# Kernel optimization log

Measured on AMD Instinct MI355X. Metric: run time of the kernel, lower is better.

The kernel has to match this reference:

```python
import jax, jax.numpy as jnp
import numpy as np

K = 20          # neighbors
T = 3           # time steps
GW = 10.0       # surrogate-gradient width
EPS = 1e-5      # batchnorm eps


def _knn_idx(f, k):
    # f: (B, N, C). torch code maximizes -||xi-xj||^2 via topk.
    x2 = jnp.sum(f * f, axis=-1)                          # (B, N)
    inner = jnp.einsum('bnc,bmc->bnm', f, f)              # (B, N, N)
    neg_d = 2.0 * inner - x2[:, :, None] - x2[:, None, :]
    return jax.lax.top_k(neg_d, k)[1]                     # (B, N, k)


def _graph_feature(f, k):
    # f: (B, N, C) -> (B, N, k, 2C) = cat(neighbor - center, neighbor)
    idx = _knn_idx(f, k)
    nb = jax.vmap(lambda ft, ix: ft[ix])(f, idx)          # (B, N, k, C)
    return jnp.concatenate([nb - f[:, :, None, :], nb], axis=-1)


def _bn(x, g, b, axes):
    # training-mode batchnorm (batch statistics), channel-last
    m = jnp.mean(x, axis=axes, keepdims=True)
    v = jnp.var(x, axis=axes, keepdims=True)
    return (x - m) * jax.lax.rsqrt(v + EPS) * g + b


def _lrelu(x):
    return jnp.where(x >= 0, x, 0.2 * x)


def _spike(x):
    # surrogate value + straight-through hard spike (training-mode detach trick)
    xc = jnp.clip(x, -10.0, 10.0)
    soft = 0.5 * jnp.exp(-0.5 * xc * xc) / np.sqrt(2.0 * np.pi) + 0.5 * jax.nn.sigmoid(GW * xc)
    hard = (x > 0).astype(x.dtype)
    return soft + jax.lax.stop_gradient(hard - soft)


def _lif(x, mem, thr, ref, md, ta, rd, tb):
    md = jnp.clip(md, 0.1, 0.99)
    ta = jnp.clip(ta, 0.001, 0.1)
    rd = jnp.clip(rd, 0.1, 0.95)
    x = x * (ref <= 0).astype(x.dtype)
    mem = mem * md * (1.0 - ref) + x
    s = _spike(mem - thr)
    mem = mem * (1.0 - s)
    ref = ref * rd + s
    thr = tb + (thr + ta * s - tb) * 0.95
    return s, mem, thr, ref


def _forward(x, W0, g0, b0, W1, g1, b1, W2, g2, b2, W3, g3, b3, Wm, gm, bm,
             l0md, l0ta, l0rd, l0tb, l1md, l1ta, l1rd, l1tb,
             l2md, l2ta, l2rd, l2tb, l3md, l3ta, l3rd, l3tb,
             lfmd, lfta, lfrd, lftb, tw):
    f0 = jnp.transpose(x, (0, 2, 1))                      # (B, N, 3)
    convs = [(W0, g0, b0), (W1, g1, b1), (W2, g2, b2), (W3, g3, b3)]
    lifs = [(l0md, l0ta, l0rd, l0tb), (l1md, l1ta, l1rd, l1tb),
            (l2md, l2ta, l2rd, l2tb), (l3md, l3ta, l3rd, l3tb)]
    states = [None] * 4
    pooled = []
    for t in range(T):
        cur = f0
        feats = []
        for i in range(4):
            gf = _graph_feature(cur, K)                   # (B, N, k, 2C)
            h = jnp.einsum('bnkc,oc->bnko', gf, convs[i][0])  # 1x1 conv
            h = _lrelu(_bn(h, convs[i][1], convs[i][2], (0, 1, 2)))
            h = jnp.max(h, axis=2)                        # max over k -> (B, N, O)
            md, ta, rd, tb = lifs[i]
            if states[i] is None:
                mem = jnp.zeros_like(h)
                thr = jnp.broadcast_to(tb, h.shape).astype(h.dtype)
                ref = jnp.zeros_like(h)
            else:
                # state manager detaches persisted states between calls
                mem, thr, ref = (jax.lax.stop_gradient(s) for s in states[i])
            s, mem, thr, ref = _lif(h, mem, thr, ref, md, ta, rd, tb)
            states[i] = (mem, thr, ref)
            feats.append(s)
            cur = s
        cat = jnp.concatenate(feats, axis=-1)             # (B, N, 960)
        agg = _lrelu(_bn(jnp.einsum('bnc,oc->bno', cat, Wm), gm, bm, (0, 1)))
        pooled.append(jnp.max(agg, axis=1))               # global max pool -> (B, 512)
    tf = jnp.stack(pooled, axis=0)                        # (T, B, 512)
    out = jnp.einsum('t,tbf->bf', jax.nn.softmax(tw), tf)
    mem = jnp.zeros_like(out)
    thr = jnp.broadcast_to(lftb, out.shape).astype(out.dtype)
    ref = jnp.zeros_like(out)
    s, _, _, _ = _lif(out, mem, thr, ref, lfmd, lfta, lfrd, lftb)
    return s


def setup_inputs() -> dict:
    key = jax.random.key(0)
    ks = iter(jax.random.split(key, 64))
    B, N = 2, 1024
    d = {}
    d['x'] = jax.random.normal(next(ks), (B, 3, N), jnp.float32)
    dims = [(64, 6), (128, 128), (256, 256), (512, 512)]  # (out, in) for 1x1 convs
    for i, (o, c) in enumerate(dims):
        d[f'W{i}'] = jax.random.normal(next(ks), (o, c), jnp.float32) / np.sqrt(c)
        d[f'g{i}'] = 1.0 + 0.1 * jax.random.normal(next(ks), (o,), jnp.float32)
        d[f'b{i}'] = 0.1 * jax.random.normal(next(ks), (o,), jnp.float32)
    d['Wm'] = jax.random.normal(next(ks), (512, 960), jnp.float32) / np.sqrt(960.0)
    d['gm'] = 1.0 + 0.1 * jax.random.normal(next(ks), (512,), jnp.float32)
    d['bm'] = 0.1 * jax.random.normal(next(ks), (512,), jnp.float32)
    for name, c in [('l0', 64), ('l1', 128), ('l2', 256), ('l3', 512), ('lf', 512)]:
        d[name + 'md'] = jnp.full((c,), 0.9, jnp.float32) + 0.02 * jax.random.normal(next(ks), (c,), jnp.float32)
        d[name + 'ta'] = jnp.full((c,), 0.01, jnp.float32) + 0.002 * jax.random.normal(next(ks), (c,), jnp.float32)
        d[name + 'rd'] = jnp.full((c,), 0.5, jnp.float32) + 0.02 * jax.random.normal(next(ks), (c,), jnp.float32)
        d[name + 'tb'] = jnp.ones((c,), jnp.float32) + 0.05 * jax.random.normal(next(ks), (c,), jnp.float32)
    d['tw'] = 1.0 + 0.1 * jax.random.normal(next(ks), (T,), jnp.float32)
    return d


def reference(x, W0, g0, b0, W1, g1, b1, W2, g2, b2, W3, g3, b3, Wm, gm, bm,
              l0md, l0ta, l0rd, l0tb, l1md, l1ta, l1rd, l1tb,
              l2md, l2ta, l2rd, l2tb, l3md, l3ta, l3rd, l3tb,
              lfmd, lfta, lfrd, lftb, tw):
    return _forward(x, W0, g0, b0, W1, g1, b1, W2, g2, b2, W3, g3, b3, Wm, gm, bm,
                    l0md, l0ta, l0rd, l0tb, l1md, l1ta, l1rd, l1tb,
                    l2md, l2ta, l2rd, l2tb, l3md, l3ta, l3rd, l3tb,
                    lfmd, lfta, lfrd, lftb, tw)
```

## Files before the change

### kernel.cpp

```cpp
#include <hip/hip_runtime.h>
#include <math.h>

#define NPTS 1024
#define BB 2
#define KNN 20
#define ROWS 2048
#define CATC 960
#define TT 3
typedef unsigned long long ull;

__device__ __forceinline__ float lrelu_f(float x){ return x >= 0.f ? x : 0.2f*x; }

__device__ __forceinline__ void gemm_dev(const float* __restrict__ A, int lda,
    const float* __restrict__ B, int ldb, float* __restrict__ C, int ldc,
    int K, int kb, int bm, int bn, int tid, float* sm)
{
  float (*As)[68] = (float(*)[68])sm;
  float (*Bs)[68] = (float(*)[68])(sm + 16*68);
  const int tx = tid & 15, ty = tid >> 4;
  const int lr = tid >> 2, kq = tid & 3;
  float acc[4][4] = {};
  if ((K & 15) == 0) {
    const float* pA = A + (size_t)(bm+lr)*lda + kb + kq*4;
    const float* pB = B + (size_t)(bn+lr)*ldb + kb + kq*4;
    float4 av = *(const float4*)pA;
    float4 bv = *(const float4*)pB;
    for (int k0 = 0; k0 < K; k0 += 16) {
      As[kq*4+0][lr]=av.x; As[kq*4+1][lr]=av.y; As[kq*4+2][lr]=av.z; As[kq*4+3][lr]=av.w;
      Bs[kq*4+0][lr]=bv.x; Bs[kq*4+1][lr]=bv.y; Bs[kq*4+2][lr]=bv.z; Bs[kq*4+3][lr]=bv.w;
      __syncthreads();
      if (k0 + 16 < K) {
        av = *(const float4*)(pA + k0 + 16);
        bv = *(const float4*)(pB + k0 + 16);
      }
#pragma unroll
      for (int kk = 0; kk < 16; ++kk) {
        float4 a4 = *(const float4*)&As[kk][ty*4];
        float4 b4 = *(const float4*)&Bs[kk][tx*4];
        float ar[4]={a4.x,a4.y,a4.z,a4.w}, br[4]={b4.x,b4.y,b4.z,b4.w};
#pragma unroll
        for (int i=0;i<4;++i)
#pragma unroll
          for (int j=0;j<4;++j) acc[i][j]=fmaf(ar[i],br[j],acc[i][j]);
      }
      __syncthreads();
    }
  } else {
    for (int k0 = 0; k0 < K; k0 += 16) {
#pragma unroll
      for (int e=0;e<4;++e){
        int gk = k0 + kq*4 + e;
        As[kq*4+e][lr] = (gk<K)? A[(size_t)(bm+lr)*lda+kb+gk] : 0.f;
        Bs[kq*4+e][lr] = (gk<K)? B[(size_t)(bn+lr)*ldb+kb+gk] : 0.f;
      }
      __syncthreads();
#pragma unroll
      for (int kk = 0; kk < 16; ++kk) {
        float4 a4 = *(const float4*)&As[kk][ty*4];
        float4 b4 = *(const float4*)&Bs[kk][tx*4];
        float ar[4]={a4.x,a4.y,a4.z,a4.w}, br[4]={b4.x,b4.y,b4.z,b4.w};
#pragma unroll
        for (int i=0;i<4;++i)
#pragma unroll
          for (int j=0;j<4;++j) acc[i][j]=fmaf(ar[i],br[j],acc[i][j]);
      }
      __syncthreads();
    }
  }
#pragma unroll
  for (int i=0;i<4;++i){
    float4 v; v.x=acc[i][0]; v.y=acc[i][1]; v.z=acc[i][2]; v.w=acc[i][3];
    *(float4*)&C[(size_t)(bm+ty*4+i)*ldc + bn + tx*4] = v;
  }
}

template<int W>
__device__ __forceinline__ void knn_wave(const ull* __restrict__ pk, int* __restrict__ idx,
                                         int row, int lane)
{
  const int n = row & (NPTS-1), b = row >> 10;
  const ull* pb = pk + (size_t)b*NPTS*W;
  ull cw[W]; int pn = 0;
#pragma unroll
  for (int w=0; w<W; ++w){ cw[w] = pb[(size_t)n*W + w]; pn += __popcll(cw[w]); }
  unsigned keys[16];
#pragma unroll 4
  for (int i=0;i<16;++i){
    int m = lane + (i<<6);
    int inner=0, pm=0;
#pragma unroll
    for (int w=0;w<W;++w){
      ull rm = pb[(size_t)m*W + w];
      inner += __popcll(rm & cw[w]);
      pm    += __popcll(rm);
    }
    int d = 2*inner - pn - pm;
    keys[i] = ((unsigned)(d+1024)<<11) | (unsigned)(NPTS-1-m);
  }
  unsigned lmax = keys[0];
#pragma unroll
  for (int i=1;i<16;++i) lmax = keys[i]>lmax ? keys[i] : lmax;
  unsigned mywin = 0;
  for (int s=0;s<KNN;++s){
    unsigned v = lmax;
#pragma unroll
    for (int off=1; off<64; off<<=1){ unsigned o = __shfl_xor(v, off, 64); if (o>v) v=o; }
    if (lane == s) mywin = (unsigned)(NPTS-1) - (v & 0x7FFu);
    if (lmax == v){
#pragma unroll
      for (int i=0;i<16;++i) if (keys[i]==v) keys[i]=0u;
      lmax = keys[0];
#pragma unroll
      for (int i=1;i<16;++i) lmax = keys[i]>lmax ? keys[i] : lmax;
    }
  }
  if (lane < KNN) idx[(size_t)row*KNN + lane] = (int)mywin;
}

__device__ __forceinline__ void knn0_wave(const float* __restrict__ x, const float* __restrict__ x2,
                                          int* __restrict__ idx, int row, int lane)
{
  const int n = row & (NPTS-1), b = row >> 10;
  const float* xb = x + (size_t)b*3*NPTS;
  float fn0 = xb[n], fn1 = xb[NPTS+n], fn2 = xb[2*NPTS+n];
  float x2n = x2[row];
  ull keys[16];
#pragma unroll 4
  for (int i=0;i<16;++i){
    int m = lane + (i<<6);
    float inner = __fadd_rn(__fadd_rn(__fmul_rn(fn0, xb[m]), __fmul_rn(fn1, xb[NPTS+m])),
                            __fmul_rn(fn2, xb[2*NPTS+m]));
    float v = __fsub_rn(__fsub_rn(__fmul_rn(2.f, inner), x2n), x2[(b<<10)+m]);
    unsigned u = __float_as_uint(v);
    u = (u & 0x80000000u) ? ~u : (u | 0x80000000u);
    keys[i] = ((ull)u << 32) | (unsigned)(NPTS-1-m);
  }
  ull lmax = keys[0];
#pragma unroll
  for (int i=1;i<16;++i) lmax = keys[i]>lmax ? keys[i] : lmax;
  unsigned mywin = 0;
  for (int s=0;s<KNN;++s){
    ull v = lmax;
#pragma unroll
    for (int off=1; off<64; off<<=1){ ull o = __shfl_xor(v, off, 64); if (o>v) v=o; }
    if (lane == s) mywin = (unsigned)(NPTS-1) - (unsigned)(v & 0xFFFFFFFFull);
    if (lmax == v){
#pragma unroll
      for (int i=0;i<16;++i) if (keys[i]==v) keys[i]=0ull;
      lmax = keys[0];
#pragma unroll
      for (int i=1;i<16;++i) lmax = keys[i]>lmax ? keys[i] : lmax;
    }
  }
  if (lane < KNN) idx[(size_t)row*KNN + lane] = (int)mywin;
}

__device__ __forceinline__ void bnlif_dev(int i, int oShift,
    const float* __restrict__ hmax, const double* __restrict__ S1, const double* __restrict__ S2,
    const float* __restrict__ g, const float* __restrict__ bb,
    const float* __restrict__ pmd, const float* __restrict__ pta,
    const float* __restrict__ prd, const float* __restrict__ ptb,
    float* __restrict__ stM, float* __restrict__ stT, float* __restrict__ stR,
    float* __restrict__ sout, int offOut, ull* __restrict__ pk, int init, int laneTid)
{
  int O = 1 << oShift;
  int bn = i >> oShift;
  int o  = i & (O - 1);
  double cnt = (double)ROWS * (double)KNN;
  double mu = S1[o] / cnt;
  double vv = S2[o] / cnt - mu*mu;
  float mean = (float)mu;
  float inv  = 1.f / sqrtf((float)vv + 1e-5f);
  float h = hmax[i];
  h = ((h - mean) * inv) * g[o] + bb[o];
  h = lrelu_f(h);
  float md = fminf(fmaxf(pmd[o], 0.1f), 0.99f);
  float ta = fminf(fmaxf(pta[o], 0.001f), 0.1f);
  float rd = fminf(fmaxf(prd[o], 0.1f), 0.95f);
  float tb = ptb[o];
  float M, T, R;
  if (init) { M = 0.f; T = tb; R = 0.f; }
  else      { M = stM[i]; T = stT[i]; R = stR[i]; }
  float xv = (R <= 0.f) ? h : 0.f;
  M = M * md * (1.f - R) + xv;
  float sp = (M - T > 0.f) ? 1.f : 0.f;
  M = M * (1.f - sp);
  R = R * rd + sp;
  T = tb + (T + ta*sp - tb) * 0.95f;
  stM[i] = M; stT[i] = T; stR[i] = R;
  sout[(size_t)bn*CATC + offOut + o] = sp;
  ull ball = __ballot(sp != 0.f);
  if ((laneTid & 63) == 0) pk[i >> 6] = ball;
}

__device__ __forceinline__ void aggfin_dev(const float* __restrict__ pA, const float* __restrict__ pB,
    const float* __restrict__ gm, const float* __restrict__ bmv, float* __restrict__ pooled,
    int o, int tid, char* smraw)
{
  double* sd1 = (double*)smraw; double* sd2 = sd1 + 256;
  float* sm0 = (float*)(sd2 + 256); float* sm1 = sm0 + 256;
  double s1=0.0, s2=0.0; float m0=-INFINITY, m1=-INFINITY;
  for (int r=tid; r<ROWS; r+=256){
    float v = __fadd_rn(pA[(size_t)r*512+o], pB[(size_t)r*512+o]);
    s1 += (double)v; s2 += (double)v*(double)v;
    if (r < NPTS) m0 = fmaxf(m0, v); else m1 = fmaxf(m1, v);
  }
  sd1[tid]=s1; sd2[tid]=s2; sm0[tid]=m0; sm1[tid]=m1;
  __syncthreads();
  for (int off=128; off>0; off>>=1){
    if (tid<off){
      sd1[tid]+=sd1[tid+off]; sd2[tid]+=sd2[tid+off];
      sm0[tid]=fmaxf(sm0[tid],sm0[tid+off]);
      sm1[tid]=fmaxf(sm1[tid],sm1[tid+off]);
    }
    __syncthreads();
  }
  if (tid==0){
    double mean = sd1[0]/(double)ROWS;
    float var = (float)(sd2[0]/(double)ROWS - mean*mean);
    float m = (float)mean;
    float inv = 1.f/sqrtf(var + 1e-5f);
    pooled[o]       = lrelu_f(((sm0[0]-m)*inv)*gm[o] + bmv[o]);
    pooled[512 + o] = lrelu_f(((sm1[0]-m)*inv)*gm[o] + bmv[o]);
  }
}

__device__ __forceinline__ void wcat_dev(const float* __restrict__ W, float* __restrict__ out,
                                         int O, int C, int i)
{
  if (i >= 2*O*C) return;
  int r = i / C, c = i - r*C;
  out[i] = (r < O) ? __fadd_rn(W[(size_t)r*2*C + c], W[(size_t)r*2*C + C + c])
                   : W[(size_t)(r-O)*2*C + c];
}

__global__ __launch_bounds__(256) void k_setup(const float* __restrict__ x,
    float* __restrict__ f0, float* __restrict__ x2,
    const float* W0, const float* W1, const float* W2, const float* W3,
    float* wc0, float* wc1, float* wc2, float* wc3, double* S12_0)
{
  int bid = blockIdx.x, tid = threadIdx.x;
  if (bid < 24) {
    int i = bid*256 + tid;
    int b = i / 3072, rem = i - b*3072, n = rem/3, c = rem - n*3;
    f0[i] = x[(size_t)b*3072 + c*NPTS + n];
  } else if (bid < 32) {
    int r = (bid-24)*256 + tid;
    int b = r >> 10, n = r & (NPTS-1);
    const float* xb = x + (size_t)b*3072;
    float a0=xb[n], a1=xb[NPTS+n], a2=xb[2*NPTS+n];
    x2[r] = __fadd_rn(__fadd_rn(__fmul_rn(a0,a0),__fmul_rn(a1,a1)),__fmul_rn(a2,a2));
  } else if (bid < 33) {
    for (int j=tid; j<1024; j+=256) S12_0[j]=0.0;
  } else if (bid < 35) {
    int i = (bid-33)*256+tid; wcat_dev(W0, wc0, 64, 3, i);
  } else if (bid < 99) {
    int i = (bid-35)*256+tid; wcat_dev(W1, wc1, 128, 64, i);
  } else if (bid < 355) {
    int i = (bid-99)*256+tid; wcat_dev(W2, wc2, 256, 128, i);
  } else {
    int i = (bid-355)*256+tid; wcat_dev(W3, wc3, 512, 256, i);
  }
}

__global__ __launch_bounds__(256) void k_nt0v2(const float* __restrict__ x, const float* __restrict__ x2,
    int* __restrict__ idx0, const float* __restrict__ f0, const float* __restrict__ wc0,
    float* __restrict__ AB)
{
  __shared__ __align__(16) float sm[2*16*68];
  int bid = blockIdx.x, tid = threadIdx.x;
  if (bid < 512) {
    knn0_wave(x, x2, idx0, bid*4 + (tid>>6), tid & 63);
  } else {
    int id = bid - 512;
    gemm_dev(f0, 3, wc0, 3, AB, 128, 3, 0, (id>>1)*64, (id&1)*64, tid, sm);
  }
}

template<int W>
__global__ __launch_bounds__(256) void k_knnconv2(const ull* __restrict__ pk, int* __restrict__ idx,
    double* __restrict__ S12, const float* __restrict__ Ain, const float* __restrict__ Bw,
    float* __restrict__ AB, int twoO, int K, int ntn)
{
  __shared__ __align__(16) float sm[2*16*68];
  int bid = blockIdx.x, tid = threadIdx.x;
  if (bid < 512) {
    if (bid == 0) { for (int j=tid; j<1024; j+=256) S12[j]=0.0; }
    knn_wave<W>(pk, idx, bid*4 + (tid>>6), tid & 63);
  } else {
    int id = bid - 512;
    int tm = id / ntn, tn = id - tm*ntn;
    gemm_dev(Ain, CATC, Bw, K, AB, twoO, K, 0, tm*64, tn*64, tid, sm);
  }
}

__global__ __launch_bounds__(256) void k_agg(const float* __restrict__ scat, const float* __restrict__ Wm,
    float* __restrict__ aggA, float* __restrict__ aggB)
{
  __shared__ __align__(16) float sm[2*16*68];
  int id = blockIdx.x;
  int part = id >> 8, tl = id & 255, tm = tl >> 3, tn = tl & 7;
  gemm_dev(scat, CATC, Wm, CATC, part ? aggB : aggA, 512, 480, part*480,
           tm*64, tn*64, threadIdx.x, sm);
}

__global__ __launch_bounds__(256) void k_lif0fin(
    const float* __restrict__ hmax0, const double* __restrict__ S1_0, const double* __restrict__ S2_0,
    const float* g, const float* bb, const float* pmd, const float* pta,
    const float* prd, const float* ptb,
    float* stM, float* stT, float* stR, float* scc, ull* pk0, int init,
    const float* aggA, const float* aggB, const float* gm, const float* bmv, float* pooled)
{
  __shared__ __align__(16) char sm[6144];
  int bid = blockIdx.x, tid = threadIdx.x;
  if (bid < 512) {
    bnlif_dev(bid*256+tid, 6, hmax0, S1_0, S2_0, g, bb, pmd, pta, prd, ptb,
              stM, stT, stR, scc, 0, pk0, init, tid);
  } else {
    aggfin_dev(aggA, aggB, gm, bmv, pooled, bid-512, tid, sm);
  }
}

__global__ __launch_bounds__(256) void k_gather(const float* __restrict__ AB, int O,
    const int* __restrict__ idx, float* __restrict__ hmax,
    double* __restrict__ S1, double* __restrict__ S2)
{
  int base = blockIdx.x * 8;
  __shared__ int sidx[8*KNN];
  for (int i = threadIdx.x; i < 8*KNN; i += blockDim.x)
    sidx[i] = idx[(size_t)base*KNN + i];
  __syncthreads();
  int twoO = 2*O;
  for (int o = threadIdx.x; o < O; o += blockDim.x) {
    double ts1 = 0.0, ts2 = 0.0;
    for (int r = 0; r < 8; ++r) {
      int bn = base + r;
      int b = bn >> 10;
      float bc = AB[(size_t)bn*twoO + O + o];
      float mx = -INFINITY;
      double s1 = 0.0, s2 = 0.0;
#pragma unroll
      for (int k = 0; k < KNN; ++k) {
        int m = sidx[r*KNN + k];
        float a = AB[((size_t)(b*NPTS + m))*twoO + o];
        mx = fmaxf(mx, a);
        s1 += (double)a;
        s2 += (double)a * (double)a;
      }
      hmax[(size_t)bn*O + o] = mx - bc;
      ts1 += s1 - (double)KNN * (double)bc;
      ts2 += s2 - 2.0*(double)bc*s1 + (double)KNN*(double)bc*(double)bc;
    }
    atomicAdd(&S1[o], ts1);
    atomicAdd(&S2[o], ts2);
  }
}

__global__ __launch_bounds__(256) void k_bnlif(const float* __restrict__ hmax, int oShift,
    const double* __restrict__ S1, const double* __restrict__ S2,
    const float* g, const float* bb, const float* pmd, const float* pta,
    const float* prd, const float* ptb,
    float* stM, float* stT, float* stR, float* scc, int offOut, ull* pk, int init)
{
  bnlif_dev(blockIdx.x*256 + threadIdx.x, oShift, hmax, S1, S2, g, bb, pmd, pta, prd, ptb,
            stM, stT, stR, scc, offOut, pk, init, threadIdx.x);
}

__global__ __launch_bounds__(256) void k_aggfin(const float* __restrict__ aggA,
    const float* __restrict__ aggB, const float* gm, const float* bmv, float* pooled)
{
  __shared__ __align__(16) char sm[6144];
  aggfin_dev(aggA, aggB, gm, bmv, pooled, blockIdx.x, threadIdx.x, sm);
}

__global__ __launch_bounds__(256) void k_final(const float* __restrict__ pooled,
    const float* __restrict__ tw, const float* __restrict__ lftb, float* __restrict__ out)
{
  int i = blockIdx.x*256 + threadIdx.x;
  if (i >= BB*512) return;
  int b = i / 512, o = i - b*512;
  float t0 = tw[0], t1 = tw[1], t2 = tw[2];
  float mx = fmaxf(t0, fmaxf(t1, t2));
  float e0 = expf(t0-mx), e1 = expf(t1-mx), e2 = expf(t2-mx);
  float den = e0 + e1 + e2;
  float v = (e0/den)*pooled[(0*BB+b)*512+o]
          + (e1/den)*pooled[(1*BB+b)*512+o]
          + (e2/den)*pooled[(2*BB+b)*512+o];
  out[i] = (v - lftb[o] > 0.f) ? 1.f : 0.f;
}

extern "C" void kernel_launch(void* const* d_in, const int* in_sizes, int n_in,
                              void* d_out, int out_size, void* d_ws, size_t ws_size,
                              hipStream_t stream)
{
  (void)in_sizes; (void)n_in; (void)out_size; (void)ws_size;
  const float* x = (const float*)d_in[0];
  const float* Wl[4] = {(const float*)d_in[1],(const float*)d_in[4],(const float*)d_in[7],(const float*)d_in[10]};
  const float* gl[4] = {(const float*)d_in[2],(const float*)d_in[5],(const float*)d_in[8],(const float*)d_in[11]};
  const float* bl[4] = {(const float*)d_in[3],(const float*)d_in[6],(const float*)d_in[9],(const float*)d_in[12]};
  const float* Wm = (const float*)d_in[13];
  const float* gm = (const float*)d_in[14];
  const float* bm = (const float*)d_in[15];
  const float* lp[5][4];
  for (int l = 0; l < 5; ++l)
    for (int q = 0; q < 4; ++q)
      lp[l][q] = (const float*)d_in[16 + l*4 + q];
  const float* tw = (const float*)d_in[36];

  char* pw = (char*)d_ws;
  auto alloc = [&](size_t bytes)->char* {
    char* r = pw; pw += (bytes + 255) & ~(size_t)255; return r;
  };
  float* f0     = (float*)alloc((size_t)ROWS*3*sizeof(float));
  float* x2     = (float*)alloc((size_t)ROWS*sizeof(float));
  int*   idx0   = (int*)  alloc((size_t)ROWS*KNN*sizeof(int));
  int*   idxS   = (int*)  alloc((size_t)ROWS*KNN*sizeof(int));
  float* AB     = (float*)alloc((size_t)ROWS*1024*sizeof(float));
  float* hmax0  = (float*)alloc((size_t)ROWS*64*sizeof(float));
  float* hmaxS  = (float*)alloc((size_t)ROWS*512*sizeof(float));
  float* aggA   = (float*)alloc((size_t)ROWS*512*sizeof(float));
  float* scat   = (float*)alloc((size_t)ROWS*CATC*sizeof(float));
  double* S12_0 = (double*)alloc(1024*sizeof(double));
  double* S12   = (double*)alloc(1024*sizeof(double));
  float* pooled = (float*)alloc((size_t)TT*BB*512*sizeof(float));
  ull* pkb[4];
  int Wn[4] = {1, 2, 4, 8};
  for (int i = 0; i < 4; ++i)
    pkb[i] = (ull*)alloc((size_t)ROWS*Wn[i]*sizeof(ull));

  int Cin[4]   = {3, 64, 128, 256};
  int Oo[4]    = {64, 128, 256, 512};
  int oSh[4]   = {6, 7, 8, 9};
  int offIn[4] = {0, 0, 64, 192};
  int offOut[4]= {0, 64, 192, 448};
  float *wcat[4], *stM[4], *stT[4], *stR[4];
  for (int i = 0; i < 4; ++i) {
    wcat[i] = (float*)alloc((size_t)2*Oo[i]*Cin[i]*sizeof(float));
    stM[i]  = (float*)alloc((size_t)ROWS*Oo[i]*sizeof(float));
    stT[i]  = (float*)alloc((size_t)ROWS*Oo[i]*sizeof(float));
    stR[i]  = (float*)alloc((size_t)ROWS*Oo[i]*sizeof(float));
  }
  double* S1_0 = S12_0; double* S2_0 = S12_0 + 512;
  double* S1 = S12;     double* S2 = S12 + 512;
  float* aggB = hmaxS;

  k_setup<<<1379, 256, 0, stream>>>(x, f0, x2, Wl[0], Wl[1], Wl[2], Wl[3],
                                    wcat[0], wcat[1], wcat[2], wcat[3], S12_0);
  k_nt0v2<<<576, 256, 0, stream>>>(x, x2, idx0, f0, wcat[0], AB);
  k_gather<<<256, 256, 0, stream>>>(AB, 64, idx0, hmax0, S1_0, S2_0);

  for (int t = 0; t < TT; ++t) {
    int init = (t == 0) ? 1 : 0;
    if (t > 0)
      k_agg<<<512, 256, 0, stream>>>(scat, Wm, aggA, aggB);
    k_lif0fin<<<(t > 0 ? 1024 : 512), 256, 0, stream>>>(
        hmax0, S1_0, S2_0, gl[0], bl[0],
        lp[0][0], lp[0][1], lp[0][2], lp[0][3],
        stM[0], stT[0], stR[0], scat, pkb[0], init,
        aggA, aggB, gm, bm, pooled + (t > 0 ? (size_t)(t-1)*BB*512 : 0));
    for (int i = 1; i < 4; ++i) {
      int C = Cin[i], O = Oo[i];
      int twoO = 2*O, ntn = twoO/64, nConv = 32*ntn;
      const float* fin = scat + offIn[i];
      switch (Wn[i-1]) {
        case 1: k_knnconv2<1><<<512+nConv, 256, 0, stream>>>(pkb[0], idxS, S12, fin, wcat[i], AB, twoO, C, ntn); break;
        case 2: k_knnconv2<2><<<512+nConv, 256, 0, stream>>>(pkb[1], idxS, S12, fin, wcat[i], AB, twoO, C, ntn); break;
        default: k_knnconv2<4><<<512+nConv, 256, 0, stream>>>(pkb[2], idxS, S12, fin, wcat[i], AB, twoO, C, ntn); break;
      }
      k_gather<<<256, 256, 0, stream>>>(AB, O, idxS, hmaxS, S1, S2);
      k_bnlif<<<(ROWS*O)/256, 256, 0, stream>>>(
          hmaxS, oSh[i], S1, S2, gl[i], bl[i],
          lp[i][0], lp[i][1], lp[i][2], lp[i][3],
          stM[i], stT[i], stR[i], scat, offOut[i], pkb[i], init);
    }
  }
  k_agg<<<512, 256, 0, stream>>>(scat, Wm, aggA, aggB);
  k_aggfin<<<512, 256, 0, stream>>>(aggA, aggB, gm, bm, pooled + (size_t)2*BB*512);
  k_final<<<4, 256, 0, stream>>>(pooled, tw, lp[4][3], (float*)d_out);
}
```

Measured before the change: 542.3 us.

## Use bf16 MFMA with three-way weight splitting for spike-input GEMMs

Replaces the fp32 shared-memory GEMMs for layers 1-3 and the aggregation projection with MFMA 16x16x32 bf16 instructions. Weights are split into three bf16 terms at setup, and spike activations, which are exactly 0 or 1, are stored as bf16, so precision is kept close to fp32. The spike concat buffer shrinks to half size. In exchange, setup work grows, each output needs three MFMA passes, operands are loaded straight from global memory without LDS staging, and the C stores are strided.

```diff
diff --git a/kernel.cpp b/kernel.cpp
--- a/kernel.cpp
+++ b/kernel.cpp
@@ -8,8 +8,18 @@
 #define CATC 960
 #define TT 3
 typedef unsigned long long ull;
+typedef __attribute__((ext_vector_type(8))) short bf16x8;
+typedef __attribute__((ext_vector_type(4))) float f32x4;
 
 __device__ __forceinline__ float lrelu_f(float x){ return x >= 0.f ? x : 0.2f*x; }
+
+__device__ __forceinline__ unsigned short f2bf(float f){
+  unsigned u = __float_as_uint(f);
+  return (unsigned short)((u + 0x7FFFu + ((u >> 16) & 1u)) >> 16);
+}
+__device__ __forceinline__ float bf2f(unsigned short h){
+  return __uint_as_float(((unsigned)h) << 16);
+}
 
 __device__ __forceinline__ void gemm_dev(const float* __restrict__ A, int lda,
     const float* __restrict__ B, int ldb, float* __restrict__ C, int ldc,
@@ -20,58 +30,64 @@
   const int tx = tid & 15, ty = tid >> 4;
   const int lr = tid >> 2, kq = tid & 3;
   float acc[4][4] = {};
-  if ((K & 15) == 0) {
-    const float* pA = A + (size_t)(bm+lr)*lda + kb + kq*4;
-    const float* pB = B + (size_t)(bn+lr)*ldb + kb + kq*4;
-    float4 av = *(const float4*)pA;
-    float4 bv = *(const float4*)pB;
-    for (int k0 = 0; k0 < K; k0 += 16) {
-      As[kq*4+0][lr]=av.x; As[kq*4+1][lr]=av.y; As[kq*4+2][lr]=av.z; As[kq*4+3][lr]=av.w;
-      Bs[kq*4+0][lr]=bv.x; Bs[kq*4+1][lr]=bv.y; Bs[kq*4+2][lr]=bv.z; Bs[kq*4+3][lr]=bv.w;
-      __syncthreads();
-      if (k0 + 16 < K) {
-        av = *(const float4*)(pA + k0 + 16);
-        bv = *(const float4*)(pB + k0 + 16);
-      }
-#pragma unroll
-      for (int kk = 0; kk < 16; ++kk) {
-        float4 a4 = *(const float4*)&As[kk][ty*4];
-        float4 b4 = *(const float4*)&Bs[kk][tx*4];
-        float ar[4]={a4.x,a4.y,a4.z,a4.w}, br[4]={b4.x,b4.y,b4.z,b4.w};
-#pragma unroll
-        for (int i=0;i<4;++i)
-#pragma unroll
-          for (int j=0;j<4;++j) acc[i][j]=fmaf(ar[i],br[j],acc[i][j]);
-      }
-      __syncthreads();
-    }
-  } else {
-    for (int k0 = 0; k0 < K; k0 += 16) {
-#pragma unroll
-      for (int e=0;e<4;++e){
-        int gk = k0 + kq*4 + e;
-        As[kq*4+e][lr] = (gk<K)? A[(size_t)(bm+lr)*lda+kb+gk] : 0.f;
-        Bs[kq*4+e][lr] = (gk<K)? B[(size_t)(bn+lr)*ldb+kb+gk] : 0.f;
-      }
-      __syncthreads();
-#pragma unroll
-      for (int kk = 0; kk < 16; ++kk) {
-        float4 a4 = *(const float4*)&As[kk][ty*4];
-        float4 b4 = *(const float4*)&Bs[kk][tx*4];
-        float ar[4]={a4.x,a4.y,a4.z,a4.w}, br[4]={b4.x,b4.y,b4.z,b4.w};
-#pragma unroll
-        for (int i=0;i<4;++i)
-#pragma unroll
-          for (int j=0;j<4;++j) acc[i][j]=fmaf(ar[i],br[j],acc[i][j]);
-      }
-      __syncthreads();
-    }
+  for (int k0 = 0; k0 < K; k0 += 16) {
+#pragma unroll
+    for (int e=0;e<4;++e){
+      int gk = k0 + kq*4 + e;
+      As[kq*4+e][lr] = (gk<K)? A[(size_t)(bm+lr)*lda+kb+gk] : 0.f;
+      Bs[kq*4+e][lr] = (gk<K)? B[(size_t)(bn+lr)*ldb+kb+gk] : 0.f;
+    }
+    __syncthreads();
+#pragma unroll
+    for (int kk = 0; kk < 16; ++kk) {
+      float4 a4 = *(const float4*)&As[kk][ty*4];
+      float4 b4 = *(const float4*)&Bs[kk][tx*4];
+      float ar[4]={a4.x,a4.y,a4.z,a4.w}, br[4]={b4.x,b4.y,b4.z,b4.w};
+#pragma unroll
+      for (int i=0;i<4;++i)
+#pragma unroll
+        for (int j=0;j<4;++j) acc[i][j]=fmaf(ar[i],br[j],acc[i][j]);
+    }
+    __syncthreads();
   }
 #pragma unroll
   for (int i=0;i<4;++i){
     float4 v; v.x=acc[i][0]; v.y=acc[i][1]; v.z=acc[i][2]; v.w=acc[i][3];
     *(float4*)&C[(size_t)(bm+ty*4+i)*ldc + bn + tx*4] = v;
   }
+}
+
+__device__ __forceinline__ void mfma_dev(const short* __restrict__ A, int lda,
+    const short* __restrict__ B3, size_t sStride, int ldb,
+    float* __restrict__ C, int ldc, int K, int kb, int bm, int bn, int tid)
+{
+  const int wave = tid >> 6, lane = tid & 63;
+  const int wm = (wave >> 1) << 5, wn = (wave & 1) << 5;
+  const int rr = lane & 15, kq = (lane >> 4) << 3;
+  f32x4 acc[2][2] = {};
+  const short* Ap = A + (size_t)(bm + wm + rr)*lda + kb + kq;
+  const short* Bp = B3 + (size_t)(bn + wn + rr)*ldb + kb + kq;
+  for (int k0 = 0; k0 < K; k0 += 32) {
+    bf16x8 a0 = *(const bf16x8*)(Ap + k0);
+    bf16x8 a1 = *(const bf16x8*)(Ap + (size_t)16*lda + k0);
+#pragma unroll
+    for (int s = 0; s < 3; ++s) {
+      bf16x8 b0 = *(const bf16x8*)(Bp + (size_t)s*sStride + k0);
+      bf16x8 b1 = *(const bf16x8*)(Bp + (size_t)s*sStride + (size_t)16*ldb + k0);
+      acc[0][0] = __builtin_amdgcn_mfma_f32_16x16x32_bf16(a0, b0, acc[0][0], 0, 0, 0);
+      acc[0][1] = __builtin_amdgcn_mfma_f32_16x16x32_bf16(a0, b1, acc[0][1], 0, 0, 0);
+      acc[1][0] = __builtin_amdgcn_mfma_f32_16x16x32_bf16(a1, b0, acc[1][0], 0, 0, 0);
+      acc[1][1] = __builtin_amdgcn_mfma_f32_16x16x32_bf16(a1, b1, acc[1][1], 0, 0, 0);
+    }
+  }
+  const int drb = (lane >> 4) << 2;
+#pragma unroll
+  for (int i = 0; i < 2; ++i)
+#pragma unroll
+    for (int j = 0; j < 2; ++j)
+#pragma unroll
+      for (int t = 0; t < 4; ++t)
+        C[(size_t)(bm + wm + i*16 + drb + t)*ldc + bn + wn + j*16 + rr] = acc[i][j][t];
 }
 
 template<int W>
@@ -161,7 +177,7 @@
     const float* __restrict__ pmd, const float* __restrict__ pta,
     const float* __restrict__ prd, const float* __restrict__ ptb,
     float* __restrict__ stM, float* __restrict__ stT, float* __restrict__ stR,
-    float* __restrict__ sout, int offOut, ull* __restrict__ pk, int init, int laneTid)
+    short* __restrict__ sout, int offOut, ull* __restrict__ pk, int init, int laneTid)
 {
   int O = 1 << oShift;
   int bn = i >> oShift;
@@ -182,13 +198,13 @@
   if (init) { M = 0.f; T = tb; R = 0.f; }
   else      { M = stM[i]; T = stT[i]; R = stR[i]; }
   float xv = (R <= 0.f) ? h : 0.f;
+  float sp = (M * md * (1.f - R) + xv - T > 0.f) ? 1.f : 0.f;
   M = M * md * (1.f - R) + xv;
-  float sp = (M - T > 0.f) ? 1.f : 0.f;
   M = M * (1.f - sp);
   R = R * rd + sp;
   T = tb + (T + ta*sp - tb) * 0.95f;
   stM[i] = M; stT[i] = T; stR[i] = R;
-  sout[(size_t)bn*CATC + offOut + o] = sp;
+  sout[(size_t)bn*CATC + offOut + o] = (sp != 0.f) ? (short)0x3F80 : (short)0;
   ull ball = __ballot(sp != 0.f);
   if ((laneTid & 63) == 0) pk[i >> 6] = ball;
 }
@@ -225,19 +241,25 @@
   }
 }
 
-__device__ __forceinline__ void wcat_dev(const float* __restrict__ W, float* __restrict__ out,
-                                         int O, int C, int i)
-{
-  if (i >= 2*O*C) return;
-  int r = i / C, c = i - r*C;
-  out[i] = (r < O) ? __fadd_rn(W[(size_t)r*2*C + c], W[(size_t)r*2*C + C + c])
-                   : W[(size_t)(r-O)*2*C + c];
+__device__ __forceinline__ void wsplit_dev(float w, short* dst, size_t NK, size_t e){
+  unsigned short h1 = f2bf(w); float f1 = bf2f(h1);
+  float r1 = w - f1;
+  unsigned short h2 = f2bf(r1); float f2v = bf2f(h2);
+  unsigned short h3 = f2bf(r1 - f2v);
+  dst[e] = (short)h1; dst[NK + e] = (short)h2; dst[2*NK + e] = (short)h3;
+}
+__device__ __forceinline__ void wcatsplit_dev(const float* __restrict__ W, short* __restrict__ dst,
+                                              int O, int C, size_t e){
+  int rr = (int)(e / C), cc = (int)(e - (size_t)rr*C);
+  float w = (rr < O) ? __fadd_rn(W[(size_t)rr*2*C + cc], W[(size_t)rr*2*C + C + cc])
+                     : W[(size_t)(rr-O)*2*C + cc];
+  wsplit_dev(w, dst, (size_t)2*O*C, e);
 }
 
 __global__ __launch_bounds__(256) void k_setup(const float* __restrict__ x,
     float* __restrict__ f0, float* __restrict__ x2,
-    const float* W0, const float* W1, const float* W2, const float* W3,
-    float* wc0, float* wc1, float* wc2, float* wc3, double* S12_0)
+    const float* W0, const float* W1, const float* W2, const float* W3, const float* Wm,
+    float* wc0, short* wcH1, short* wcH2, short* wcH3, short* WmH, double* S12_0)
 {
   int bid = blockIdx.x, tid = threadIdx.x;
   if (bid < 24) {
@@ -253,14 +275,16 @@
   } else if (bid < 33) {
     for (int j=tid; j<1024; j+=256) S12_0[j]=0.0;
   } else if (bid < 35) {
-    int i = (bid-33)*256+tid; wcat_dev(W0, wc0, 64, 3, i);
-  } else if (bid < 99) {
-    int i = (bid-35)*256+tid; wcat_dev(W1, wc1, 128, 64, i);
-  } else if (bid < 355) {
-    int i = (bid-99)*256+tid; wcat_dev(W2, wc2, 256, 128, i);
-  } else {
-    int i = (bid-355)*256+tid; wcat_dev(W3, wc3, 512, 256, i);
-  }
+    int i = (bid-33)*256+tid;
+    if (i < 2*64*3){
+      int r = i/3, c = i-r*3;
+      wc0[i] = (r<64) ? __fadd_rn(W0[(size_t)r*6+c], W0[(size_t)r*6+3+c])
+                      : W0[(size_t)(r-64)*6+c];
+    }
+  } else if (bid < 99)   { wcatsplit_dev(W1, wcH1, 128,  64, (size_t)(bid-35)*256+tid); }
+  else if (bid < 355)    { wcatsplit_dev(W2, wcH2, 256, 128, (size_t)(bid-99)*256+tid); }
+  else if (bid < 1379)   { wcatsplit_dev(W3, wcH3, 512, 256, (size_t)(bid-355)*256+tid); }
+  else                   { size_t e = (size_t)(bid-1379)*256+tid; wsplit_dev(Wm[e], WmH, (size_t)512*960, e); }
 }
 
 __global__ __launch_bounds__(256) void k_nt0v2(const float* __restrict__ x, const float* __restrict__ x2,
@@ -278,11 +302,10 @@
 }
 
 template<int W>
-__global__ __launch_bounds__(256) void k_knnconv2(const ull* __restrict__ pk, int* __restrict__ idx,
-    double* __restrict__ S12, const float* __restrict__ Ain, const float* __restrict__ Bw,
-    float* __restrict__ AB, int twoO, int K, int ntn)
-{
-  __shared__ __align__(16) float sm[2*16*68];
+__global__ __launch_bounds__(256) void k_knnmfma(const ull* __restrict__ pk, int* __restrict__ idx,
+    double* __restrict__ S12, const short* __restrict__ Ain, const short* __restrict__ B3,
+    size_t sStride, float* __restrict__ AB, int twoO, int K, int ntn)
+{
   int bid = blockIdx.x, tid = threadIdx.x;
   if (bid < 512) {
     if (bid == 0) { for (int j=tid; j<1024; j+=256) S12[j]=0.0; }
@@ -290,25 +313,24 @@
   } else {
     int id = bid - 512;
     int tm = id / ntn, tn = id - tm*ntn;
-    gemm_dev(Ain, CATC, Bw, K, AB, twoO, K, 0, tm*64, tn*64, tid, sm);
-  }
-}
-
-__global__ __launch_bounds__(256) void k_agg(const float* __restrict__ scat, const float* __restrict__ Wm,
-    float* __restrict__ aggA, float* __restrict__ aggB)
-{
-  __shared__ __align__(16) float sm[2*16*68];
+    mfma_dev(Ain, CATC, B3, sStride, K, AB, twoO, K, 0, tm*64, tn*64, tid);
+  }
+}
+
+__global__ __launch_bounds__(256) void k_aggmfma(const short* __restrict__ scatH,
+    const short* __restrict__ WmH, float* __restrict__ aggA, float* __restrict__ aggB)
+{
   int id = blockIdx.x;
   int part = id >> 8, tl = id & 255, tm = tl >> 3, tn = tl & 7;
-  gemm_dev(scat, CATC, Wm, CATC, part ? aggB : aggA, 512, 480, part*480,
-           tm*64, tn*64, threadIdx.x, sm);
+  mfma_dev(scatH, CATC, WmH, (size_t)512*960, 960, part ? aggB : aggA, 512,
+           480, part*480, tm*64, tn*64, threadIdx.x);
 }
 
 __global__ __launch_bounds__(256) void k_lif0fin(
     const float* __restrict__ hmax0, const double* __restrict__ S1_0, const double* __restrict__ S2_0,
     const float* g, const float* bb, const float* pmd, const float* pta,
     const float* prd, const float* ptb,
-    float* stM, float* stT, float* stR, float* scc, ull* pk0, int init,
+    float* stM, float* stT, float* stR, short* scc, ull* pk0, int init,
     const float* aggA, const float* aggB, const float* gm, const float* bmv, float* pooled)
 {
   __shared__ __align__(16) char sm[6144];
@@ -360,7 +382,7 @@
     const double* __restrict__ S1, const double* __restrict__ S2,
     const float* g, const float* bb, const float* pmd, const float* pta,
     const float* prd, const float* ptb,
-    float* stM, float* stT, float* stR, float* scc, int offOut, ull* pk, int init)
+    float* stM, float* stT, float* stR, short* scc, int offOut, ull* pk, int init)
 {
   bnlif_dev(blockIdx.x*256 + threadIdx.x, oShift, hmax, S1, S2, g, bb, pmd, pta, prd, ptb,
             stM, stT, stR, scc, offOut, pk, init, threadIdx.x);
@@ -419,7 +441,7 @@
   float* hmax0  = (float*)alloc((size_t)ROWS*64*sizeof(float));
   float* hmaxS  = (float*)alloc((size_t)ROWS*512*sizeof(float));
   float* aggA   = (float*)alloc((size_t)ROWS*512*sizeof(float));
-  float* scat   = (float*)alloc((size_t)ROWS*CATC*sizeof(float));
+  short* scatH  = (short*)alloc((size_t)ROWS*CATC*sizeof(short));
   double* S12_0 = (double*)alloc(1024*sizeof(double));
   double* S12   = (double*)alloc(1024*sizeof(double));
   float* pooled = (float*)alloc((size_t)TT*BB*512*sizeof(float));
@@ -433,9 +455,14 @@
   int oSh[4]   = {6, 7, 8, 9};
   int offIn[4] = {0, 0, 64, 192};
   int offOut[4]= {0, 64, 192, 448};
-  float *wcat[4], *stM[4], *stT[4], *stR[4];
+  float* wc0 = (float*)alloc((size_t)2*64*3*sizeof(float));
+  short* wcH[4];
+  wcH[1] = (short*)alloc((size_t)3*256*64*sizeof(short));
+  wcH[2] = (short*)alloc((size_t)3*512*128*sizeof(short));
+  wcH[3] = (short*)alloc((size_t)3*1024*256*sizeof(short));
+  short* WmH = (short*)alloc((size_t)3*512*960*sizeof(short));
+  float *stM[4], *stT[4], *stR[4];
   for (int i = 0; i < 4; ++i) {
-    wcat[i] = (float*)alloc((size_t)2*Oo[i]*Cin[i]*sizeof(float));
     stM[i]  = (float*)alloc((size_t)ROWS*Oo[i]*sizeof(float));
     stT[i]  = (float*)alloc((size_t)ROWS*Oo[i]*sizeof(float));
     stR[i]  = (float*)alloc((size_t)ROWS*Oo[i]*sizeof(float));
@@ -444,37 +471,38 @@
   double* S1 = S12;     double* S2 = S12 + 512;
   float* aggB = hmaxS;
 
-  k_setup<<<1379, 256, 0, stream>>>(x, f0, x2, Wl[0], Wl[1], Wl[2], Wl[3],
-                                    wcat[0], wcat[1], wcat[2], wcat[3], S12_0);
-  k_nt0v2<<<576, 256, 0, stream>>>(x, x2, idx0, f0, wcat[0], AB);
+  k_setup<<<3299, 256, 0, stream>>>(x, f0, x2, Wl[0], Wl[1], Wl[2], Wl[3], Wm,
+                                    wc0, wcH[1], wcH[2], wcH[3], WmH, S12_0);
+  k_nt0v2<<<576, 256, 0, stream>>>(x, x2, idx0, f0, wc0, AB);
   k_gather<<<256, 256, 0, stream>>>(AB, 64, idx0, hmax0, S1_0, S2_0);
 
   for (int t = 0; t < TT; ++t) {
     int init = (t == 0) ? 1 : 0;
     if (t > 0)
-      k_agg<<<512, 256, 0, stream>>>(scat, Wm, aggA, aggB);
+      k_aggmfma<<<512, 256, 0, stream>>>(scatH, WmH, aggA, aggB);
     k_lif0fin<<<(t > 0 ? 1024 : 512), 256, 0, stream>>>(
         hmax0, S1_0, S2_0, gl[0], bl[0],
         lp[0][0], lp[0][1], lp[0][2], lp[0][3],
-        stM[0], stT[0], stR[0], scat, pkb[0], init,
+        stM[0], stT[0], stR[0], scatH, pkb[0], init,
         aggA, aggB, gm, bm, pooled + (t > 0 ? (size_t)(t-1)*BB*512 : 0));
     for (int i = 1; i < 4; ++i) {
       int C = Cin[i], O = Oo[i];
       int twoO = 2*O, ntn = twoO/64, nConv = 32*ntn;
-      const float* fin = scat + offIn[i];
+      const short* fin = scatH + offIn[i];
+      size_t sStr = (size_t)twoO*C;
       switch (Wn[i-1]) {
-        case 1: k_knnconv2<1><<<512+nConv, 256, 0, stream>>>(pkb[0], idxS, S12, fin, wcat[i], AB, twoO, C, ntn); break;
-        case 2: k_knnconv2<2><<<512+nConv, 256, 0, stream>>>(pkb[1], idxS, S12, fin, wcat[i], AB, twoO, C, ntn); break;
-        default: k_knnconv2<4><<<512+nConv, 256, 0, stream>>>(pkb[2], idxS, S12, fin, wcat[i], AB, twoO, C, ntn); break;
+        case 1: k_knnmfma<1><<<512+nConv, 256, 0, stream>>>(pkb[0], idxS, S12, fin, wcH[i], sStr, AB, twoO, C, ntn); break;
+        case 2: k_knnmfma<2><<<512+nConv, 256, 0, stream>>>(pkb[1], idxS, S12, fin, wcH[i], sStr, AB, twoO, C, ntn); break;
+        default: k_knnmfma<4><<<512+nConv, 256, 0, stream>>>(pkb[2], idxS, S12, fin, wcH[i], sStr, AB, twoO, C, ntn); break;
       }
       k_gather<<<256, 256, 0, stream>>>(AB, O, idxS, hmaxS, S1, S2);
       k_bnlif<<<(ROWS*O)/256, 256, 0, stream>>>(
           hmaxS, oSh[i], S1, S2, gl[i], bl[i],
           lp[i][0], lp[i][1], lp[i][2], lp[i][3],
-          stM[i], stT[i], stR[i], scat, offOut[i], pkb[i], init);
-    }
-  }
-  k_agg<<<512, 256, 0, stream>>>(scat, Wm, aggA, aggB);
+          stM[i], stT[i], stR[i], scatH, offOut[i], pkb[i], init);
+    }
+  }
+  k_aggmfma<<<512, 256, 0, stream>>>(scatH, WmH, aggA, aggB);
   k_aggfin<<<512, 256, 0, stream>>>(aggA, aggB, gm, bm, pooled + (size_t)2*BB*512);
   k_final<<<4, 256, 0, stream>>>(pooled, tw, lp[4][3], (float*)d_out);
 }
```

Result: no change. 545.7 us (+0.6%).
